# Performance work log

Hardware: AMD Instinct MI355X
Metric: run time of the kernel (lower is better)

Reference implementation:

```python
import jax, jax.numpy as jnp
import numpy as np

N_NODES = 100000
N_EDGES = 1600000
VOCAB = 2048
NODE_DIM = 64
HIDDEN = 64
N_MASK = 10000


def setup_inputs() -> dict:
    key = jax.random.key(0)
    ks = jax.random.split(key, 10)
    x = jax.random.randint(ks[0], (N_NODES, 1), 0, VOCAB, dtype=jnp.int64)
    edge_index = jax.random.randint(ks[1], (2, N_EDGES), 0, N_NODES, dtype=jnp.int64)
    mask_x_position = jax.random.randint(ks[2], (N_MASK,), 0, N_NODES, dtype=jnp.int64)
    # embedding init: normal with std = node_dim ** -0.5 (as in initialize_parameters)
    emb = jax.random.normal(ks[3], (VOCAB, NODE_DIM), dtype=jnp.float32) * (NODE_DIM ** -0.5)
    # SAGEConv layer 1: lin_l (neighbors, with bias), lin_r (root, no bias)
    s1 = (NODE_DIM ** -0.5)
    W_l1 = jax.random.uniform(ks[4], (NODE_DIM, HIDDEN), jnp.float32, -s1, s1)
    b_l1 = jnp.zeros((HIDDEN,), jnp.float32)
    W_r1 = jax.random.uniform(ks[5], (NODE_DIM, HIDDEN), jnp.float32, -s1, s1)
    # SAGEConv layer 2
    s2 = (HIDDEN ** -0.5)
    W_l2 = jax.random.uniform(ks[6], (HIDDEN, VOCAB), jnp.float32, -s2, s2)
    b_l2 = jnp.zeros((VOCAB,), jnp.float32)
    W_r2 = jax.random.uniform(ks[7], (HIDDEN, VOCAB), jnp.float32, -s2, s2)
    return {"x": x, "edge_index": edge_index, "mask_x_position": mask_x_position,
            "emb": emb, "W_l1": W_l1, "b_l1": b_l1, "W_r1": W_r1,
            "W_l2": W_l2, "b_l2": b_l2, "W_r2": W_r2}


def _sage_conv(h, src, dst, W_l, b_l, W_r):
    # mean-aggregate source-node features at destination nodes (PyG SAGEConv, aggr='mean')
    msgs = h[src]                                                  # [E, D]
    agg = jax.ops.segment_sum(msgs, dst, num_segments=N_NODES)     # [N, D]
    deg = jax.ops.segment_sum(jnp.ones((src.shape[0], 1), h.dtype), dst,
                              num_segments=N_NODES)                # [N, 1]
    mean = agg / jnp.maximum(deg, 1.0)
    return mean @ W_l + b_l + h @ W_r


def reference(x, edge_index, mask_x_position, emb, W_l1, b_l1, W_r1, W_l2, b_l2, W_r2):
    src, dst = edge_index[0], edge_index[1]
    h = emb[x[:, 0]]                                # embedding(x).squeeze(1) -> [N, node_dim]
    # dropout is identity in eval mode
    h = _sage_conv(h, src, dst, W_l1, b_l1, W_r1)   # [N, hidden]
    h = jax.nn.relu(h)
    h = _sage_conv(h, src, dst, W_l2, b_l2, W_r2)   # [N, vocab]
    return jax.nn.log_softmax(h[mask_x_position], axis=1)
```

## Files before the change

kernel.cpp:

```cpp
#include <hip/hip_runtime.h>
#include <math.h>

#define N_NODES   100000
#define N_EDGES   1600000
#define VOCAB     2048
#define NODE_DIM  64
#define HIDDEN    64
#define N_MASK    10000

#define BN        96
#define NBKT      1042
#define CHUNK     2048
#define NCH       782
#define ELCAP     2048

typedef __attribute__((ext_vector_type(8))) short short8;
typedef __attribute__((ext_vector_type(4))) float f32x4;
typedef unsigned short ushort_t;
typedef unsigned int uint_t;

#define H1_OFF      0
#define ESRC_OFF    25600000
#define E2_OFF      32000000
#define EWL_OFF     44800000
#define EWR_OFF     45324288
#define W2T_OFF     45848576
#define X2B_OFF     46372864
#define ROWPTR_OFF  48932864
#define BCNT_OFF    49332880
#define BPTR_OFF    49337056
#define MAT_OFF     49341232

__device__ __forceinline__ ushort_t f2bf(float f) {
    uint_t u = __builtin_bit_cast(uint_t, f);
    u += 0x7FFFu + ((u >> 16) & 1u);
    return (ushort_t)(u >> 16);
}

__global__ __launch_bounds__(256) void k_prep(const float* __restrict__ emb,
                                              const float* __restrict__ Wl1,
                                              const float* __restrict__ Wr1,
                                              const float* __restrict__ Wl2,
                                              const float* __restrict__ Wr2,
                                              float* __restrict__ embWl,
                                              float* __restrict__ embWr,
                                              ushort_t* __restrict__ W2T) {
    __shared__ ushort_t T[64 * 66];
    const int bx = blockIdx.x;
    const int tid = threadIdx.x;
    if (bx < 1024) {
        const int half = bx >> 9;
        const float* W = half ? Wr1 : Wl1;
        float* out = half ? embWr : embWl;
        int idx = (bx & 511) * 256 + tid;
        int v = idx >> 6, c = idx & 63;
        float s = 0.0f;
#pragma unroll 8
        for (int k = 0; k < 64; k++) s += emb[v * 64 + k] * W[k * 64 + c];
        out[idx] = s;
    } else {
        int t = bx - 1024;
        const int k0 = (t & 1) * 64;
        const int n0 = (t >> 1) * 64;
        const float* Wsrc = (k0 == 0) ? Wl2 : Wr2;
#pragma unroll
        for (int i = 0; i < 16; i++) {
            int idx = i * 256 + tid;
            int k = idx >> 6, n = idx & 63;
            T[n * 66 + k] = f2bf(Wsrc[(size_t)k * VOCAB + n0 + n]);
        }
        __syncthreads();
#pragma unroll
        for (int i = 0; i < 16; i++) {
            int idx = i * 256 + tid;
            int n = idx >> 6, k = idx & 63;
            W2T[(size_t)(n0 + n) * 128 + k0 + k] = T[n * 66 + k];
        }
    }
}

__global__ __launch_bounds__(256) void k_count2(const int* __restrict__ dst,
                                                ushort_t* __restrict__ mat) {
    __shared__ int hist[NBKT];
    const int c = blockIdx.x, t = threadIdx.x;
    const int e0 = c * CHUNK;
    const int n = min(CHUNK, N_EDGES - e0);
    for (int i = t; i < NBKT; i += 256) hist[i] = 0;
    int d[8];
#pragma unroll
    for (int i = 0; i < 8; i++) {
        int idx = i * 256 + t;
        d[i] = (idx < n) ? dst[e0 + idx] : -1;
    }
    __syncthreads();
#pragma unroll
    for (int i = 0; i < 8; i++)
        if (d[i] >= 0) atomicAdd(&hist[d[i] / BN], 1);
    __syncthreads();
    for (int i = t; i < NBKT; i += 256) mat[(size_t)c * NBKT + i] = (ushort_t)hist[i];
}

__global__ __launch_bounds__(1024) void k_mscan(ushort_t* __restrict__ mat,
                                                int* __restrict__ bcnt) {
    __shared__ int s[1024];
    const int b = blockIdx.x, t = threadIdx.x;
    int v = (t < NCH) ? (int)mat[(size_t)t * NBKT + b] : 0;
    s[t] = v;
    __syncthreads();
    for (int off = 1; off < 1024; off <<= 1) {
        int a = (t >= off) ? s[t - off] : 0;
        __syncthreads();
        s[t] += a;
        __syncthreads();
    }
    if (t < NCH) mat[(size_t)t * NBKT + b] = (ushort_t)(s[t] - v);
    if (t == NCH - 1) bcnt[b] = s[t];
}

__global__ __launch_bounds__(1024) void k_bscan(const int* __restrict__ bcnt,
                                                int* __restrict__ bptr,
                                                int* __restrict__ rowptr) {
    __shared__ int s[1024];
    int t = threadIdx.x;
    int i0 = 2 * t, i1 = 2 * t + 1;
    int a = (i0 < NBKT) ? bcnt[i0] : 0;
    int b = (i1 < NBKT) ? bcnt[i1] : 0;
    int v = a + b;
    s[t] = v;
    __syncthreads();
    for (int off = 1; off < 1024; off <<= 1) {
        int p = (t >= off) ? s[t - off] : 0;
        __syncthreads();
        s[t] += p;
        __syncthreads();
    }
    int excl = s[t] - v;
    if (i0 < NBKT) bptr[i0] = excl;
    if (i1 < NBKT) bptr[i1] = excl + a;
    if (t == 1023) bptr[NBKT] = s[t];
    if (t == 0) rowptr[N_NODES] = N_EDGES;
}

__global__ __launch_bounds__(256) void k_scatter3(const int* __restrict__ src,
                                                  const int* __restrict__ dst,
                                                  const int* __restrict__ x,
                                                  const ushort_t* __restrict__ mat,
                                                  const int* __restrict__ bptr,
                                                  int2* __restrict__ e2) {
    __shared__ int cur[NBKT];
    const int c = blockIdx.x, t = threadIdx.x;
    const int e0 = c * CHUNK;
    const int n = min(CHUNK, N_EDGES - e0);
    for (int i = t; i < NBKT; i += 256)
        cur[i] = bptr[i] + (int)mat[(size_t)c * NBKT + i];
    int d[8], sv[8], voc[8];
#pragma unroll
    for (int i = 0; i < 8; i++) {
        int idx = i * 256 + t;
        if (idx < n) { d[i] = dst[e0 + idx]; sv[i] = src[e0 + idx]; }
        else d[i] = -1;
    }
#pragma unroll
    for (int i = 0; i < 8; i++)
        if (d[i] >= 0) voc[i] = x[sv[i]];
    __syncthreads();
#pragma unroll
    for (int i = 0; i < 8; i++) {
        if (d[i] >= 0) {
            int b = d[i] / BN;
            int pos = atomicAdd(&cur[b], 1);
            e2[pos] = make_int2(sv[i], (voc[i] << 8) | (d[i] - b * BN));
        }
    }
}

__global__ __launch_bounds__(512) void k_sortagg(const int* __restrict__ bptr,
                                                 const int2* __restrict__ e2,
                                                 const int* __restrict__ x,
                                                 const float* __restrict__ embWl,
                                                 const float* __restrict__ embWr,
                                                 const float* __restrict__ b1,
                                                 int* __restrict__ rowptr,
                                                 int* __restrict__ esrc,
                                                 float* __restrict__ h1) {
    __shared__ int2 eL[ELCAP];
    __shared__ int sc[128];
    __shared__ int cur[BN];
    __shared__ int base[BN + 1];
    const int b = blockIdx.x;
    const int t = threadIdx.x;
    const int r0 = bptr[b], r1 = bptr[b + 1];
    const int m = r1 - r0;

    if (t < 128) sc[t] = 0;
    __syncthreads();
    for (int i = t; i < m; i += 512)
        atomicAdd(&sc[e2[r0 + i].y & 255], 1);
    __syncthreads();
    int v = (t < 128) ? sc[t] : 0;
    for (int off = 1; off < 128; off <<= 1) {
        int a = (t >= off && t < 128) ? sc[t - off] : 0;
        __syncthreads();
        if (t < 128) sc[t] += a;
        __syncthreads();
    }
    if (t < BN) {
        int excl = sc[t] - v;
        base[t] = excl;
        cur[t] = excl;
        int node = b * BN + t;
        if (node < N_NODES) rowptr[node] = r0 + excl;
        if (t == BN - 1) base[BN] = sc[t];
    }
    __syncthreads();
    for (int i = t; i < m; i += 512) {
        int2 ev = e2[r0 + i];
        int pos = atomicAdd(&cur[ev.y & 255], 1);
        eL[pos] = ev;
    }
    __syncthreads();
    for (int i = t; i < m; i += 512)
        esrc[r0 + i] = eL[i].x;

    const int wv = t >> 6, lane = t & 63;
    const float b1v = b1[lane];
    for (int nl = wv; nl < BN; nl += 8) {
        int node = b * BN + nl;
        if (node >= N_NODES) break;
        int j0 = base[nl], j1 = base[nl + 1];
        int deg = j1 - j0;
        float s0 = 0.0f, s1 = 0.0f, s2 = 0.0f, s3 = 0.0f;
        int j = j0;
        for (; j + 3 < j1; j += 4) {
            int va = eL[j].y >> 8;
            int vb = eL[j + 1].y >> 8;
            int vc = eL[j + 2].y >> 8;
            int vd = eL[j + 3].y >> 8;
            s0 += embWl[(va << 6) + lane];
            s1 += embWl[(vb << 6) + lane];
            s2 += embWl[(vc << 6) + lane];
            s3 += embWl[(vd << 6) + lane];
        }
        for (; j < j1; j++)
            s0 += embWl[((eL[j].y >> 8) << 6) + lane];
        float sum = (s0 + s1) + (s2 + s3);
        float inv = 1.0f / fmaxf((float)deg, 1.0f);
        float self = embWr[(x[node] << 6) + lane];
        h1[((size_t)node << 6) + lane] = fmaxf(sum * inv + self + b1v, 0.0f);
    }
}

__global__ __launch_bounds__(256) void k_x2(const int* __restrict__ mask,
                                            const int* __restrict__ rowptr,
                                            const int* __restrict__ esrc,
                                            const float* __restrict__ h1,
                                            ushort_t* __restrict__ X2b) {
    int gw = (blockIdx.x * 256 + threadIdx.x) >> 6;
    int lane = threadIdx.x & 63;
    if (gw >= N_MASK) return;
    int n = mask[gw];
    int r0 = rowptr[n], r1 = rowptr[n + 1];
    int deg = r1 - r0;
    float s0 = 0.0f, s1 = 0.0f, s2 = 0.0f, s3 = 0.0f;
    for (int base = 0; base < deg; base += 64) {
        int cnt = min(64, deg - base);
        int mys = (base + lane < deg) ? esrc[r0 + base + lane] : 0;
        int t = 0;
        for (; t + 3 < cnt; t += 4) {
            int sa = __shfl(mys, t);
            int sb = __shfl(mys, t + 1);
            int sc = __shfl(mys, t + 2);
            int sd = __shfl(mys, t + 3);
            s0 += h1[((size_t)sa << 6) + lane];
            s1 += h1[((size_t)sb << 6) + lane];
            s2 += h1[((size_t)sc << 6) + lane];
            s3 += h1[((size_t)sd << 6) + lane];
        }
        for (; t < cnt; t++)
            s0 += h1[((size_t)__shfl(mys, t) << 6) + lane];
    }
    float sum = (s0 + s1) + (s2 + s3);
    float inv = 1.0f / fmaxf((float)deg, 1.0f);
    X2b[gw * 128 + lane]      = f2bf(sum * inv);
    X2b[gw * 128 + 64 + lane] = f2bf(h1[((size_t)n << 6) + lane]);
}

__global__ __launch_bounds__(256) void k_gemm2_mfma(const ushort_t* __restrict__ X2b,
                                                    const ushort_t* __restrict__ W2T,
                                                    const float* __restrict__ bias,
                                                    float* __restrict__ out,
                                                    int M) {
    __shared__ ushort_t As[64 * 144];
    __shared__ ushort_t Bs[64 * 144];
    const int tid  = threadIdx.x;
    const int row0 = blockIdx.x * 64;
    const int col0 = blockIdx.y * 64;

#pragma unroll
    for (int i = 0; i < 4; i++) {
        int idx = i * 256 + tid;
        int r = idx >> 4, ch = idx & 15;
        int R = row0 + r;
        short8 v = {0, 0, 0, 0, 0, 0, 0, 0};
        if (R < M) v = *(const short8*)(X2b + (size_t)R * 128 + ch * 8);
        *(short8*)(As + r * 144 + ch * 8) = v;
    }
#pragma unroll
    for (int i = 0; i < 4; i++) {
        int idx = i * 256 + tid;
        int r = idx >> 4, ch = idx & 15;
        *(short8*)(Bs + r * 144 + ch * 8) =
            *(const short8*)(W2T + (size_t)(col0 + r) * 128 + ch * 8);
    }
    __syncthreads();

    const int lane = tid & 63;
    const int wv   = tid >> 6;
    const int wr = wv >> 1, wc = wv & 1;
    const int l15 = lane & 15, q = lane >> 4;

    f32x4 acc[2][2] = {};
    const ushort_t* Abase = As + (wr * 32 + l15) * 144 + q * 8;
    const ushort_t* Bbase = Bs + (wc * 32 + l15) * 144 + q * 8;

#pragma unroll
    for (int ks = 0; ks < 4; ks++) {
        short8 a0 = *(const short8*)(Abase + ks * 32);
        short8 a1 = *(const short8*)(Abase + 16 * 144 + ks * 32);
        short8 b0 = *(const short8*)(Bbase + ks * 32);
        short8 b1 = *(const short8*)(Bbase + 16 * 144 + ks * 32);
        acc[0][0] = __builtin_amdgcn_mfma_f32_16x16x32_bf16(a0, b0, acc[0][0], 0, 0, 0);
        acc[0][1] = __builtin_amdgcn_mfma_f32_16x16x32_bf16(a0, b1, acc[0][1], 0, 0, 0);
        acc[1][0] = __builtin_amdgcn_mfma_f32_16x16x32_bf16(a1, b0, acc[1][0], 0, 0, 0);
        acc[1][1] = __builtin_amdgcn_mfma_f32_16x16x32_bf16(a1, b1, acc[1][1], 0, 0, 0);
    }

#pragma unroll
    for (int ni = 0; ni < 2; ni++) {
        int c_ = col0 + wc * 32 + ni * 16 + l15;
        float bv = bias[c_];
#pragma unroll
        for (int mi = 0; mi < 2; mi++) {
#pragma unroll
            for (int reg = 0; reg < 4; reg++) {
                int r_ = row0 + wr * 32 + mi * 16 + q * 4 + reg;
                if (r_ < M) out[(size_t)r_ * VOCAB + c_] = acc[mi][ni][reg] + bv;
            }
        }
    }
}

__global__ __launch_bounds__(256) void k_logsoftmax(float* __restrict__ out) {
    const int row = blockIdx.x;
    float4* p4 = (float4*)(out + (size_t)row * VOCAB);
    const int tid = threadIdx.x;
    float4 v[2];
    float m = -INFINITY;
#pragma unroll
    for (int i = 0; i < 2; i++) {
        v[i] = p4[tid + i * 256];
        m = fmaxf(m, fmaxf(fmaxf(v[i].x, v[i].y), fmaxf(v[i].z, v[i].w)));
    }
#pragma unroll
    for (int off = 1; off < 64; off <<= 1) m = fmaxf(m, __shfl_xor(m, off));
    __shared__ float redm[4];
    __shared__ float reds[4];
    int wave = tid >> 6;
    if ((tid & 63) == 0) redm[wave] = m;
    __syncthreads();
    m = fmaxf(fmaxf(redm[0], redm[1]), fmaxf(redm[2], redm[3]));
    float s = 0.0f;
#pragma unroll
    for (int i = 0; i < 2; i++)
        s += expf(v[i].x - m) + expf(v[i].y - m) + expf(v[i].z - m) + expf(v[i].w - m);
#pragma unroll
    for (int off = 1; off < 64; off <<= 1) s += __shfl_xor(s, off);
    if ((tid & 63) == 0) reds[wave] = s;
    __syncthreads();
    s = reds[0] + reds[1] + reds[2] + reds[3];
    float L = m + logf(s);
#pragma unroll
    for (int i = 0; i < 2; i++) {
        float4 o = v[i];
        o.x -= L; o.y -= L; o.z -= L; o.w -= L;
        p4[tid + i * 256] = o;
    }
}

extern "C" void kernel_launch(void* const* d_in, const int* in_sizes, int n_in,
                              void* d_out, int out_size, void* d_ws, size_t ws_size,
                              hipStream_t stream) {
    const int*   x    = (const int*)d_in[0];
    const int*   ei   = (const int*)d_in[1];
    const int*   src  = ei;
    const int*   dst  = ei + N_EDGES;
    const int*   mask = (const int*)d_in[2];
    const float* emb  = (const float*)d_in[3];
    const float* Wl1  = (const float*)d_in[4];
    const float* bl1  = (const float*)d_in[5];
    const float* Wr1  = (const float*)d_in[6];
    const float* Wl2  = (const float*)d_in[7];
    const float* bl2  = (const float*)d_in[8];
    const float* Wr2  = (const float*)d_in[9];
    float* out = (float*)d_out;

    char* ws = (char*)d_ws;
    float*    h1     = (float*)(ws + H1_OFF);
    int*      esrc   = (int*)(ws + ESRC_OFF);
    int2*     e2     = (int2*)(ws + E2_OFF);
    float*    embWl  = (float*)(ws + EWL_OFF);
    float*    embWr  = (float*)(ws + EWR_OFF);
    ushort_t* W2T    = (ushort_t*)(ws + W2T_OFF);
    ushort_t* X2b    = (ushort_t*)(ws + X2B_OFF);
    int*      rowptr = (int*)(ws + ROWPTR_OFF);
    int*      bcnt   = (int*)(ws + BCNT_OFF);
    int*      bptr   = (int*)(ws + BPTR_OFF);
    ushort_t* mat    = (ushort_t*)(ws + MAT_OFF);

    k_count2  <<<NCH, 256, 0, stream>>>(dst, mat);
    k_mscan   <<<NBKT, 1024, 0, stream>>>(mat, bcnt);
    k_bscan   <<<1, 1024, 0, stream>>>(bcnt, bptr, rowptr);
    k_scatter3<<<NCH, 256, 0, stream>>>(src, dst, x, mat, bptr, e2);

    k_prep<<<1088, 256, 0, stream>>>(emb, Wl1, Wr1, Wl2, Wr2, embWl, embWr, W2T);

    k_sortagg<<<NBKT, 512, 0, stream>>>(bptr, e2, x, embWl, embWr, bl1, rowptr, esrc, h1);

    k_x2<<<(N_MASK * 64 + 255) / 256, 256, 0, stream>>>(mask, rowptr, esrc, h1, X2b);
    dim3 g2((N_MASK + 63) / 64, VOCAB / 64);
    k_gemm2_mfma<<<g2, 256, 0, stream>>>(X2b, W2T, bl2, out, N_MASK);

    k_logsoftmax<<<N_MASK, 256, 0, stream>>>(out);
}
```

Measured before the change: 264.0 us.

## Replace per-bucket CSR sort with shared-memory atomic accumulation for both aggregations

Removes the in-bucket counting sort that built rowptr/esrc. Layer-1 aggregation now accumulates embWl rows into a per-bucket LDS accumulator with shared atomics. Layer-2 aggregation for masked nodes rescans the bucketed edge list, using a mask-to-row map to keep only edges whose destination is masked, and a final kernel gathers the results. This drops the sort and the esrc write, but adds many LDS float atomics, a second full pass over all edges, and a memset plus mask-map scatter.

Result: slower. 953.2 us (+261.0%).

```diff
diff --git a/kernel.cpp b/kernel.cpp
--- a/kernel.cpp
+++ b/kernel.cpp
@@ -12,7 +12,6 @@
 #define NBKT      1042
 #define CHUNK     2048
 #define NCH       782
-#define ELCAP     2048
 
 typedef __attribute__((ext_vector_type(8))) short short8;
 typedef __attribute__((ext_vector_type(4))) float f32x4;
@@ -20,16 +19,17 @@
 typedef unsigned int uint_t;
 
 #define H1_OFF      0
-#define ESRC_OFF    25600000
-#define E2_OFF      32000000
-#define EWL_OFF     44800000
-#define EWR_OFF     45324288
-#define W2T_OFF     45848576
-#define X2B_OFF     46372864
-#define ROWPTR_OFF  48932864
-#define BCNT_OFF    49332880
-#define BPTR_OFF    49337056
-#define MAT_OFF     49341232
+#define E2_OFF      25600000
+#define EWL_OFF     38400000
+#define EWR_OFF     38924288
+#define W2T_OFF     39448576
+#define X2B_OFF     39972864
+#define X2S_OFF     42532864
+#define MMAP_OFF    43812864
+#define IDEG_OFF    44212864
+#define BCNT_OFF    44612864
+#define BPTR_OFF    44617040
+#define MAT_OFF     44621216
 
 __device__ __forceinline__ ushort_t f2bf(float f) {
     uint_t u = __builtin_bit_cast(uint_t, f);
@@ -42,9 +42,11 @@
                                               const float* __restrict__ Wr1,
                                               const float* __restrict__ Wl2,
                                               const float* __restrict__ Wr2,
+                                              const int* __restrict__ mask,
                                               float* __restrict__ embWl,
                                               float* __restrict__ embWr,
-                                              ushort_t* __restrict__ W2T) {
+                                              ushort_t* __restrict__ W2T,
+                                              int* __restrict__ maskmap) {
     __shared__ ushort_t T[64 * 66];
     const int bx = blockIdx.x;
     const int tid = threadIdx.x;
@@ -58,7 +60,7 @@
 #pragma unroll 8
         for (int k = 0; k < 64; k++) s += emb[v * 64 + k] * W[k * 64 + c];
         out[idx] = s;
-    } else {
+    } else if (bx < 1088) {
         int t = bx - 1024;
         const int k0 = (t & 1) * 64;
         const int n0 = (t >> 1) * 64;
@@ -76,6 +78,9 @@
             int n = idx >> 6, k = idx & 63;
             W2T[(size_t)(n0 + n) * 128 + k0 + k] = T[n * 66 + k];
         }
+    } else {
+        int i = (bx - 1088) * 256 + tid;
+        if (i < N_MASK) maskmap[mask[i]] = i;
     }
 }
 
@@ -118,8 +123,7 @@
 }
 
 __global__ __launch_bounds__(1024) void k_bscan(const int* __restrict__ bcnt,
-                                                int* __restrict__ bptr,
-                                                int* __restrict__ rowptr) {
+                                                int* __restrict__ bptr) {
     __shared__ int s[1024];
     int t = threadIdx.x;
     int i0 = 2 * t, i1 = 2 * t + 1;
@@ -138,7 +142,6 @@
     if (i0 < NBKT) bptr[i0] = excl;
     if (i1 < NBKT) bptr[i1] = excl + a;
     if (t == 1023) bptr[NBKT] = s[t];
-    if (t == 0) rowptr[N_NODES] = N_EDGES;
 }
 
 __global__ __launch_bounds__(256) void k_scatter3(const int* __restrict__ src,
@@ -174,115 +177,118 @@
     }
 }
 
-__global__ __launch_bounds__(512) void k_sortagg(const int* __restrict__ bptr,
-                                                 const int2* __restrict__ e2,
-                                                 const int* __restrict__ x,
-                                                 const float* __restrict__ embWl,
-                                                 const float* __restrict__ embWr,
-                                                 const float* __restrict__ b1,
-                                                 int* __restrict__ rowptr,
-                                                 int* __restrict__ esrc,
-                                                 float* __restrict__ h1) {
-    __shared__ int2 eL[ELCAP];
-    __shared__ int sc[128];
-    __shared__ int cur[BN];
-    __shared__ int base[BN + 1];
+__global__ __launch_bounds__(512) void k_agg1b(const int* __restrict__ bptr,
+                                               const int2* __restrict__ e2,
+                                               const int* __restrict__ x,
+                                               const float* __restrict__ embWl,
+                                               const float* __restrict__ embWr,
+                                               const float* __restrict__ b1,
+                                               float* __restrict__ h1,
+                                               float* __restrict__ invdeg) {
+    __shared__ float acc[BN * 64];
+    __shared__ int degc[BN];
     const int b = blockIdx.x;
     const int t = threadIdx.x;
     const int r0 = bptr[b], r1 = bptr[b + 1];
-    const int m = r1 - r0;
-
-    if (t < 128) sc[t] = 0;
-    __syncthreads();
-    for (int i = t; i < m; i += 512)
-        atomicAdd(&sc[e2[r0 + i].y & 255], 1);
-    __syncthreads();
-    int v = (t < 128) ? sc[t] : 0;
-    for (int off = 1; off < 128; off <<= 1) {
-        int a = (t >= off && t < 128) ? sc[t - off] : 0;
-        __syncthreads();
-        if (t < 128) sc[t] += a;
-        __syncthreads();
-    }
-    if (t < BN) {
-        int excl = sc[t] - v;
-        base[t] = excl;
-        cur[t] = excl;
-        int node = b * BN + t;
-        if (node < N_NODES) rowptr[node] = r0 + excl;
-        if (t == BN - 1) base[BN] = sc[t];
-    }
-    __syncthreads();
-    for (int i = t; i < m; i += 512) {
-        int2 ev = e2[r0 + i];
-        int pos = atomicAdd(&cur[ev.y & 255], 1);
-        eL[pos] = ev;
-    }
-    __syncthreads();
-    for (int i = t; i < m; i += 512)
-        esrc[r0 + i] = eL[i].x;
-
     const int wv = t >> 6, lane = t & 63;
+
+    for (int i = t; i < BN * 64; i += 512) acc[i] = 0.0f;
+    if (t < BN) degc[t] = 0;
+    __syncthreads();
+
+    for (int base = r0 + wv * 64; base < r1; base += 512) {
+        int cnt = min(64, r1 - base);
+        int2 ev = (lane < cnt) ? e2[base + lane] : make_int2(0, 0);
+        if (lane < cnt) atomicAdd(&degc[ev.y & 255], 1);
+        int tt = 0;
+        for (; tt + 3 < cnt; tt += 4) {
+            int ya = __shfl(ev.y, tt);
+            int yb = __shfl(ev.y, tt + 1);
+            int yc = __shfl(ev.y, tt + 2);
+            int yd = __shfl(ev.y, tt + 3);
+            float fa = embWl[((ya >> 8) << 6) + lane];
+            float fb = embWl[((yb >> 8) << 6) + lane];
+            float fc = embWl[((yc >> 8) << 6) + lane];
+            float fd = embWl[((yd >> 8) << 6) + lane];
+            atomicAdd(&acc[(ya & 255) * 64 + lane], fa);
+            atomicAdd(&acc[(yb & 255) * 64 + lane], fb);
+            atomicAdd(&acc[(yc & 255) * 64 + lane], fc);
+            atomicAdd(&acc[(yd & 255) * 64 + lane], fd);
+        }
+        for (; tt < cnt; tt++) {
+            int y_ = __shfl(ev.y, tt);
+            atomicAdd(&acc[(y_ & 255) * 64 + lane], embWl[((y_ >> 8) << 6) + lane]);
+        }
+    }
+    __syncthreads();
+
     const float b1v = b1[lane];
     for (int nl = wv; nl < BN; nl += 8) {
         int node = b * BN + nl;
         if (node >= N_NODES) break;
-        int j0 = base[nl], j1 = base[nl + 1];
-        int deg = j1 - j0;
-        float s0 = 0.0f, s1 = 0.0f, s2 = 0.0f, s3 = 0.0f;
-        int j = j0;
-        for (; j + 3 < j1; j += 4) {
-            int va = eL[j].y >> 8;
-            int vb = eL[j + 1].y >> 8;
-            int vc = eL[j + 2].y >> 8;
-            int vd = eL[j + 3].y >> 8;
-            s0 += embWl[(va << 6) + lane];
-            s1 += embWl[(vb << 6) + lane];
-            s2 += embWl[(vc << 6) + lane];
-            s3 += embWl[(vd << 6) + lane];
-        }
-        for (; j < j1; j++)
-            s0 += embWl[((eL[j].y >> 8) << 6) + lane];
-        float sum = (s0 + s1) + (s2 + s3);
-        float inv = 1.0f / fmaxf((float)deg, 1.0f);
+        float inv = 1.0f / fmaxf((float)degc[nl], 1.0f);
         float self = embWr[(x[node] << 6) + lane];
-        h1[((size_t)node << 6) + lane] = fmaxf(sum * inv + self + b1v, 0.0f);
-    }
-}
-
-__global__ __launch_bounds__(256) void k_x2(const int* __restrict__ mask,
-                                            const int* __restrict__ rowptr,
-                                            const int* __restrict__ esrc,
-                                            const float* __restrict__ h1,
-                                            ushort_t* __restrict__ X2b) {
+        h1[((size_t)node << 6) + lane] = fmaxf(acc[nl * 64 + lane] * inv + self + b1v, 0.0f);
+        if (lane == 0) invdeg[node] = inv;
+    }
+}
+
+__global__ __launch_bounds__(512) void k_x2b(const int* __restrict__ bptr,
+                                             const int2* __restrict__ e2,
+                                             const int* __restrict__ maskmap,
+                                             const float* __restrict__ invdeg,
+                                             const float* __restrict__ h1,
+                                             ushort_t* __restrict__ X2s) {
+    __shared__ float acc2[BN * 64];
+    __shared__ int flagL[BN];
+    const int b = blockIdx.x;
+    const int t = threadIdx.x;
+    const int r0 = bptr[b], r1 = bptr[b + 1];
+    const int wv = t >> 6, lane = t & 63;
+
+    for (int i = t; i < BN * 64; i += 512) acc2[i] = 0.0f;
+    if (t < BN) {
+        int node = b * BN + t;
+        flagL[t] = (node < N_NODES) ? maskmap[node] : -1;
+    }
+    __syncthreads();
+
+    for (int base = r0 + wv * 64; base < r1; base += 512) {
+        int cnt = min(64, r1 - base);
+        int2 ev = (lane < cnt) ? e2[base + lane] : make_int2(0, 0);
+        bool fl = (lane < cnt) && (flagL[ev.y & 255] >= 0);
+        unsigned long long bal = __ballot(fl);
+        while (bal) {
+            int tt = __builtin_ctzll(bal);
+            bal &= bal - 1;
+            int y_ = __shfl(ev.y, tt);
+            int s_ = __shfl(ev.x, tt);
+            atomicAdd(&acc2[(y_ & 255) * 64 + lane], h1[((size_t)s_ << 6) + lane]);
+        }
+    }
+    __syncthreads();
+
+    for (int nl = wv; nl < BN; nl += 8) {
+        int rep = flagL[nl];
+        if (rep < 0) continue;
+        int node = b * BN + nl;
+        float iv = invdeg[node];
+        X2s[(size_t)rep * 64 + lane] = f2bf(acc2[nl * 64 + lane] * iv);
+    }
+}
+
+__global__ __launch_bounds__(256) void k_x2fin(const int* __restrict__ mask,
+                                               const int* __restrict__ maskmap,
+                                               const ushort_t* __restrict__ X2s,
+                                               const float* __restrict__ h1,
+                                               ushort_t* __restrict__ X2b) {
     int gw = (blockIdx.x * 256 + threadIdx.x) >> 6;
     int lane = threadIdx.x & 63;
     if (gw >= N_MASK) return;
-    int n = mask[gw];
-    int r0 = rowptr[n], r1 = rowptr[n + 1];
-    int deg = r1 - r0;
-    float s0 = 0.0f, s1 = 0.0f, s2 = 0.0f, s3 = 0.0f;
-    for (int base = 0; base < deg; base += 64) {
-        int cnt = min(64, deg - base);
-        int mys = (base + lane < deg) ? esrc[r0 + base + lane] : 0;
-        int t = 0;
-        for (; t + 3 < cnt; t += 4) {
-            int sa = __shfl(mys, t);
-            int sb = __shfl(mys, t + 1);
-            int sc = __shfl(mys, t + 2);
-            int sd = __shfl(mys, t + 3);
-            s0 += h1[((size_t)sa << 6) + lane];
-            s1 += h1[((size_t)sb << 6) + lane];
-            s2 += h1[((size_t)sc << 6) + lane];
-            s3 += h1[((size_t)sd << 6) + lane];
-        }
-        for (; t < cnt; t++)
-            s0 += h1[((size_t)__shfl(mys, t) << 6) + lane];
-    }
-    float sum = (s0 + s1) + (s2 + s3);
-    float inv = 1.0f / fmaxf((float)deg, 1.0f);
-    X2b[gw * 128 + lane]      = f2bf(sum * inv);
-    X2b[gw * 128 + 64 + lane] = f2bf(h1[((size_t)n << 6) + lane]);
+    int node = mask[gw];
+    int rep = maskmap[node];
+    X2b[gw * 128 + lane]      = X2s[(size_t)rep * 64 + lane];
+    X2b[gw * 128 + 64 + lane] = f2bf(h1[((size_t)node << 6) + lane]);
 }
 
 __global__ __launch_bounds__(256) void k_gemm2_mfma(const ushort_t* __restrict__ X2b,
@@ -406,27 +412,31 @@
 
     char* ws = (char*)d_ws;
     float*    h1     = (float*)(ws + H1_OFF);
-    int*      esrc   = (int*)(ws + ESRC_OFF);
     int2*     e2     = (int2*)(ws + E2_OFF);
     float*    embWl  = (float*)(ws + EWL_OFF);
     float*    embWr  = (float*)(ws + EWR_OFF);
     ushort_t* W2T    = (ushort_t*)(ws + W2T_OFF);
     ushort_t* X2b    = (ushort_t*)(ws + X2B_OFF);
-    int*      rowptr = (int*)(ws + ROWPTR_OFF);
+    ushort_t* X2s    = (ushort_t*)(ws + X2S_OFF);
+    int*      maskmap= (int*)(ws + MMAP_OFF);
+    float*    invdeg = (float*)(ws + IDEG_OFF);
     int*      bcnt   = (int*)(ws + BCNT_OFF);
     int*      bptr   = (int*)(ws + BPTR_OFF);
     ushort_t* mat    = (ushort_t*)(ws + MAT_OFF);
 
+    hipMemsetAsync(ws + MMAP_OFF, 0xFF, 400000, stream);
+
     k_count2  <<<NCH, 256, 0, stream>>>(dst, mat);
     k_mscan   <<<NBKT, 1024, 0, stream>>>(mat, bcnt);
-    k_bscan   <<<1, 1024, 0, stream>>>(bcnt, bptr, rowptr);
+    k_bscan   <<<1, 1024, 0, stream>>>(bcnt, bptr);
     k_scatter3<<<NCH, 256, 0, stream>>>(src, dst, x, mat, bptr, e2);
 
-    k_prep<<<1088, 256, 0, stream>>>(emb, Wl1, Wr1, Wl2, Wr2, embWl, embWr, W2T);
-
-    k_sortagg<<<NBKT, 512, 0, stream>>>(bptr, e2, x, embWl, embWr, bl1, rowptr, esrc, h1);
-
-    k_x2<<<(N_MASK * 64 + 255) / 256, 256, 0, stream>>>(mask, rowptr, esrc, h1, X2b);
+    k_prep<<<1128, 256, 0, stream>>>(emb, Wl1, Wr1, Wl2, Wr2, mask, embWl, embWr, W2T, maskmap);
+
+    k_agg1b<<<NBKT, 512, 0, stream>>>(bptr, e2, x, embWl, embWr, bl1, h1, invdeg);
+
+    k_x2b<<<NBKT, 512, 0, stream>>>(bptr, e2, maskmap, invdeg, h1, X2s);
+    k_x2fin<<<(N_MASK * 64 + 255) / 256, 256, 0, stream>>>(mask, maskmap, X2s, h1, X2b);
     dim3 g2((N_MASK + 63) / 64, VOCAB / 64);
     k_gemm2_mfma<<<g2, 256, 0, stream>>>(X2b, W2T, bl2, out, N_MASK);
 
```
